# Optimization experiments

Hardware: AMD Instinct MI355X
Metric: run time of the kernel (lower is better)

The kernel has to match this reference:

```python
import jax, jax.numpy as jnp
import numpy as np

DIM = 2048
N_HEADS = 16
Q_LORA = 1536
KV_LORA = 512
NOPE = 128
ROPE = 64
V_HEAD = 128
QK_HEAD = NOPE + ROPE  # 192
B, S = 2, 2048
SCALE = QK_HEAD ** -0.5
EPS = 1e-6


def rmsnorm(x, w):
    return x * jax.lax.rsqrt(jnp.mean(x * x, axis=-1, keepdims=True) + EPS) * w


def apply_rope(x, cos, sin):
    # x: [b, s, h, d]; cos/sin: [s, d//2]; complex multiply on interleaved pairs
    xr = x.reshape(x.shape[:-1] + (-1, 2))
    c = cos[None, :, None, :]
    s = sin[None, :, None, :]
    re = xr[..., 0] * c - xr[..., 1] * s
    im = xr[..., 0] * s + xr[..., 1] * c
    return jnp.stack([re, im], axis=-1).reshape(x.shape)


def setup_inputs() -> dict:
    key = jax.random.key(0)
    ks = jax.random.split(key, 8)
    w = 0.02
    x = jax.random.normal(ks[0], (B, S, DIM), dtype=jnp.float32)
    # rotary tables
    inv_freq = 1.0 / (10000.0 ** (np.arange(0, ROPE, 2, dtype=np.float32) / ROPE))
    ang = np.arange(S, dtype=np.float32)[:, None] * inv_freq[None, :]
    freqs_cos = jnp.asarray(np.cos(ang))
    freqs_sin = jnp.asarray(np.sin(ang))
    # causal mask (upper triangular large-negative)
    mask = jnp.triu(jnp.full((S, S), -1e9, dtype=jnp.float32), k=1)
    return {
        "x": x,
        "freqs_cos": freqs_cos,
        "freqs_sin": freqs_sin,
        "mask": mask,
        "wq_a": w * jax.random.normal(ks[1], (Q_LORA, DIM), dtype=jnp.float32),
        "q_norm_w": jnp.ones((Q_LORA,), dtype=jnp.float32),
        "wq_b": w * jax.random.normal(ks[2], (N_HEADS * QK_HEAD, Q_LORA), dtype=jnp.float32),
        "wkv_a": w * jax.random.normal(ks[3], (KV_LORA + ROPE, DIM), dtype=jnp.float32),
        "kv_norm_w": jnp.ones((KV_LORA,), dtype=jnp.float32),
        "wkv_b": w * jax.random.normal(ks[4], (N_HEADS * (NOPE + V_HEAD), KV_LORA), dtype=jnp.float32),
        "wo": w * jax.random.normal(ks[5], (DIM, N_HEADS * V_HEAD), dtype=jnp.float32),
    }


def reference(x, freqs_cos, freqs_sin, mask, wq_a, q_norm_w, wq_b, wkv_a, kv_norm_w, wkv_b, wo):
    b, s, _ = x.shape
    # q low-rank path
    q = rmsnorm(x @ wq_a.T, q_norm_w) @ wq_b.T
    q = q.reshape(b, s, N_HEADS, QK_HEAD)
    q_nope, q_pe = q[..., :NOPE], q[..., NOPE:]
    q_pe = apply_rope(q_pe, freqs_cos, freqs_sin)
    # kv latent + decoupled rope key
    kv = x @ wkv_a.T
    c, k_pe = kv[..., :KV_LORA], kv[..., KV_LORA:]
    k_pe = apply_rope(k_pe[:, :, None, :], freqs_cos, freqs_sin)[:, :, 0, :]  # [b,t,r]
    # absorption: fold W^UK into q
    wkvb = wkv_b.reshape(N_HEADS, NOPE + V_HEAD, KV_LORA)
    q_abs = jnp.einsum("bshd,hdc->bshc", q_nope, wkvb[:, :NOPE])
    kv_cache = rmsnorm(c, kv_norm_w)  # [b,t,c] (start_pos=0 prefill)
    # scores over latent + rope parts, fp32 softmax
    scores = (jnp.einsum("bshc,btc->bsht", q_abs, kv_cache)
              + jnp.einsum("bshr,btr->bsht", q_pe, k_pe)) * SCALE
    scores = scores + mask[:, None, :]
    p = jax.nn.softmax(scores.astype(jnp.float32), axis=-1)
    # attend in latent space, then project out with W^UV
    o = jnp.einsum("bsht,btc->bshc", p, kv_cache)
    o = jnp.einsum("bshc,hdc->bshd", o, wkvb[:, -V_HEAD:])
    return o.reshape(b, s, N_HEADS * V_HEAD) @ wo.T
```

## Files before the change

kernel.cpp:

```cpp
#include <hip/hip_runtime.h>

typedef __bf16        bf16x8 __attribute__((ext_vector_type(8)));
typedef float         f32x4  __attribute__((ext_vector_type(4)));

typedef unsigned int __attribute__((address_space(1))) as1_u32;
typedef unsigned int __attribute__((address_space(3))) as3_u32;
#define ASYNC16(gp, lp) __builtin_amdgcn_global_load_lds((as1_u32*)(gp), (as3_u32*)(lp), 16, 0, 0)

#define SCALE_F 0.07216878364870323f
#define LOG2E_F 1.4426950408889634f
#define FQ (SCALE_F * LOG2E_F)

static __device__ __forceinline__ unsigned short f2bf(float f) {
  unsigned int u = __builtin_bit_cast(unsigned int, f);
  u += 0x7fff + ((u >> 16) & 1);
  return (unsigned short)(u >> 16);
}
static __device__ __forceinline__ float bf2f(unsigned short s) {
  unsigned int u = ((unsigned int)s) << 16;
  return __builtin_bit_cast(float, u);
}

__global__ __launch_bounds__(256) void k_f2b(const float* __restrict__ in,
                                             unsigned short* __restrict__ out, int n) {
  int stride = gridDim.x * 256;
  for (int i = blockIdx.x * 256 + threadIdx.x; i < n; i += stride) out[i] = f2bf(in[i]);
}

__global__ __launch_bounds__(256) void k_wkvb(const float* __restrict__ wkvb,
                                              unsigned short* __restrict__ w_nt,
                                              unsigned short* __restrict__ w_v) {
  int i = blockIdx.x * 256 + threadIdx.x;
  int h = i >> 16;
  int rem = i & 65535;
  int c = rem >> 7, d = rem & 127;
  w_nt[i] = f2bf(wkvb[((h << 8) + d) * 512 + c]);
  int d2 = rem >> 9, c2 = rem & 511;
  w_v[i] = f2bf(wkvb[((h << 8) + 128 + d2) * 512 + c2]);
}

template <int BF16_OUT>
__global__ __launch_bounds__(256) void k_gemm(
    const unsigned short* __restrict__ A, int lda, long long sA,
    const unsigned short* __restrict__ W, int ldw, long long sW,
    void* __restrict__ Cv, int ldc, long long sC, int K) {
  __shared__ unsigned short lA[128 * 32];
  __shared__ unsigned short lW[128 * 32];
  const int tid = threadIdx.x;
  const int lane = tid & 63;
  const int q4 = lane >> 4, c16 = lane & 15;
  const int wave = tid >> 6;
  const int wr = (wave >> 1) * 64, wc = (wave & 1) * 64;
  const int z = blockIdx.z;
  A += (long long)z * sA;
  W += (long long)z * sW;

  f32x4 acc[4][4];
#pragma unroll
  for (int i = 0; i < 4; i++)
#pragma unroll
    for (int j = 0; j < 4; j++) acc[i][j] = (f32x4)0.0f;

  const int r = tid >> 2;
  const int cc = (tid & 3) * 8;
  const unsigned short* gA0 = A + ((long long)blockIdx.y * 128 + r) * lda + cc;
  const unsigned short* gA1 = gA0 + (long long)64 * lda;
  const unsigned short* gW0 = W + ((long long)blockIdx.x * 128 + r) * ldw + cc;
  const unsigned short* gW1 = gW0 + (long long)64 * ldw;
  unsigned short* pA0 = &lA[r * 32 + cc];
  unsigned short* pA1 = &lA[(64 + r) * 32 + cc];
  unsigned short* pW0 = &lW[r * 32 + cc];
  unsigned short* pW1 = &lW[(64 + r) * 32 + cc];

  for (int k0 = 0; k0 < K; k0 += 32) {
    ASYNC16(gA0 + k0, pA0);
    ASYNC16(gA1 + k0, pA1);
    ASYNC16(gW0 + k0, pW0);
    ASYNC16(gW1 + k0, pW1);
    __syncthreads();
    bf16x8 af[4], wf[4];
#pragma unroll
    for (int mt = 0; mt < 4; mt++)
      af[mt] = *(const bf16x8*)&lA[(wr + mt * 16 + c16) * 32 + q4 * 8];
#pragma unroll
    for (int nt = 0; nt < 4; nt++)
      wf[nt] = *(const bf16x8*)&lW[(wc + nt * 16 + c16) * 32 + q4 * 8];
#pragma unroll
    for (int mt = 0; mt < 4; mt++)
#pragma unroll
      for (int nt = 0; nt < 4; nt++)
        acc[mt][nt] = __builtin_amdgcn_mfma_f32_16x16x32_bf16(af[mt], wf[nt], acc[mt][nt], 0, 0, 0);
    __syncthreads();
  }

  const long long row0 = (long long)blockIdx.y * 128 + wr + q4 * 4;
  const int col0 = blockIdx.x * 128 + wc + c16;
  if (BF16_OUT) {
    unsigned short* C = (unsigned short*)Cv + (long long)z * sC;
#pragma unroll
    for (int mt = 0; mt < 4; mt++)
#pragma unroll
      for (int i = 0; i < 4; i++) {
        long long rr = (row0 + mt * 16 + i) * (long long)ldc + col0;
#pragma unroll
        for (int nt = 0; nt < 4; nt++) C[rr + nt * 16] = f2bf(acc[mt][nt][i]);
      }
  } else {
    float* C = (float*)Cv + (long long)z * sC;
#pragma unroll
    for (int mt = 0; mt < 4; mt++)
#pragma unroll
      for (int i = 0; i < 4; i++) {
        long long rr = (row0 + mt * 16 + i) * (long long)ldc + col0;
#pragma unroll
        for (int nt = 0; nt < 4; nt++) C[rr + nt * 16] = acc[mt][nt][i];
      }
  }
}

__global__ __launch_bounds__(256) void k_rms_q(const float* __restrict__ in,
                                               const float* __restrict__ w,
                                               unsigned short* __restrict__ out) {
  const int row = blockIdx.x;
  const int tid = threadIdx.x;
  const float* x = in + (long long)row * 1536;
  float v[6], ss = 0.f;
#pragma unroll
  for (int i = 0; i < 6; i++) { v[i] = x[tid + i * 256]; ss += v[i] * v[i]; }
#pragma unroll
  for (int d = 1; d < 64; d <<= 1) ss += __shfl_xor(ss, d);
  __shared__ float red[4];
  if ((tid & 63) == 0) red[tid >> 6] = ss;
  __syncthreads();
  float sc = rsqrtf((red[0] + red[1] + red[2] + red[3]) * (1.0f / 1536.0f) + 1e-6f);
#pragma unroll
  for (int i = 0; i < 6; i++)
    out[(long long)row * 1536 + tid + i * 256] = f2bf(v[i] * sc * w[tid + i * 256]);
}

__global__ __launch_bounds__(256) void k_prep_kv(const float* __restrict__ kvf,
                                                 const float* __restrict__ wn,
                                                 const float* __restrict__ fc,
                                                 const float* __restrict__ fs,
                                                 unsigned short* __restrict__ kvk,
                                                 unsigned short* __restrict__ kvt) {
  const int row = blockIdx.x;
  const int tid = threadIdx.x;
  const float* x = kvf + (long long)row * 640;
  float v0 = x[tid], v1 = x[tid + 256];
  float ss = v0 * v0 + v1 * v1;
#pragma unroll
  for (int d = 1; d < 64; d <<= 1) ss += __shfl_xor(ss, d);
  __shared__ float red[4];
  if ((tid & 63) == 0) red[tid >> 6] = ss;
  __syncthreads();
  float sc = rsqrtf((red[0] + red[1] + red[2] + red[3]) * (1.0f / 512.0f) + 1e-6f);
  const int b = row >> 11, t = row & 2047, tt = t >> 5, tl = t & 31;
  float y0 = v0 * sc * wn[tid], y1 = v1 * sc * wn[tid + 256];
  unsigned short* kb = kvk + (long long)(b * 64 + tt) * 18432;
  unsigned short* vb = kvt + (long long)(b * 64 + tt) * 16384;
  const int d0 = tid, d1 = tid + 256;
  kb[((d0 >> 3) * 32 + tl) * 8 + (d0 & 7)] = f2bf(y0);
  kb[((d1 >> 3) * 32 + tl) * 8 + (d1 & 7)] = f2bf(y1);
  vb[((tl >> 3) * 512 + d0) * 8 + (tl & 7)] = f2bf(y0);
  vb[((tl >> 3) * 512 + d1) * 8 + (tl & 7)] = f2bf(y1);
  if (tid < 32) {
    float x0 = x[512 + 2 * tid], x1 = x[513 + 2 * tid];
    float c = fc[t * 32 + tid], s = fs[t * 32 + tid];
    const int e0 = 512 + 2 * tid, e1 = e0 + 1;
    kb[((e0 >> 3) * 32 + tl) * 8 + (e0 & 7)] = f2bf(x0 * c - x1 * s);
    kb[((e1 >> 3) * 32 + tl) * 8 + (e1 & 7)] = f2bf(x0 * s + x1 * c);
  }
}

__global__ __launch_bounds__(256) void k_repack(const unsigned short* __restrict__ q,
                                                const float* __restrict__ fc,
                                                const float* __restrict__ fs,
                                                unsigned short* __restrict__ qnp,
                                                unsigned short* __restrict__ qcat) {
  const int h = blockIdx.y;
  const int row = blockIdx.x * 4 + (threadIdx.x >> 6);
  const int ln = threadIdx.x & 63;
  const unsigned short* src = q + (long long)row * 3072 + h * 192;
  unsigned short* dn = qnp + ((long long)h * 4096 + row) * 128;
  dn[ln] = f2bf(bf2f(src[ln]) * FQ);
  dn[ln + 64] = f2bf(bf2f(src[ln + 64]) * FQ);
  if (ln < 32) {
    const int t = row & 2047;
    float x0 = bf2f(src[128 + 2 * ln]), x1 = bf2f(src[129 + 2 * ln]);
    float c = fc[t * 32 + ln], s = fs[t * 32 + ln];
    unsigned short* dc = qcat + ((long long)h * 4096 + row) * 576 + 512;
    dc[2 * ln] = f2bf((x0 * c - x1 * s) * FQ);
    dc[2 * ln + 1] = f2bf((x0 * s + x1 * c) * FQ);
  }
}

__global__ __launch_bounds__(256, 2) void k_attn(const unsigned short* __restrict__ qcat,
                                                 const unsigned short* __restrict__ kvk,
                                                 const unsigned short* __restrict__ kvt,
                                                 unsigned short* __restrict__ opk) {
  __shared__ unsigned short kt[18432];
  __shared__ unsigned short vt[16384];
  __shared__ unsigned short pl[4][16][32];
  const int tid = threadIdx.x, lane = tid & 63, wave = tid >> 6;
  const int q4 = lane >> 4, c16 = lane & 15;
  const int pair = blockIdx.x, h = blockIdx.y, b = blockIdx.z;
  const unsigned short* kvk_b = kvk + (long long)b * 64 * 18432;
  const unsigned short* kvt_b = kvt + (long long)b * 64 * 16384;

  bf16x8 ones;
#pragma unroll
  for (int i = 0; i < 8; i++) ones[i] = (__bf16)1.0f;

  for (int seg = 0; seg < 2; seg++) {
    const int qt = seg ? (31 - pair) : pair;
    const int s_wave = qt * 64 + wave * 16;
    const long long qrow = (long long)h * 4096 + b * 2048 + s_wave;

    bf16x8 qf[18];
    {
      const unsigned short* qp = qcat + (qrow + c16) * 576 + q4 * 8;
#pragma unroll
      for (int kc = 0; kc < 18; kc++) qf[kc] = *(const bf16x8*)(qp + kc * 32);
    }
    f32x4 oacc[32];
#pragma unroll
    for (int i = 0; i < 32; i++) oacc[i] = (f32x4)0.f;
    f32x4 lacc = (f32x4)0.f;

    const int nT = (qt + 1) * 2;
    for (int tt = 0; tt < nT; tt++) {
      const int t0 = tt * 32;
      const unsigned short* kg = kvk_b + (long long)tt * 18432;
      const unsigned short* vg = kvt_b + (long long)tt * 16384;
#pragma unroll
      for (int i = 0; i < 9; i++) { int ch = i * 256 + tid; ASYNC16(kg + ch * 8, &kt[ch * 8]); }
#pragma unroll
      for (int i = 0; i < 8; i++) { int ch = i * 256 + tid; ASYNC16(vg + ch * 8, &vt[ch * 8]); }
      __syncthreads();

      f32x4 s0 = (f32x4)0.f, s1 = (f32x4)0.f;
#pragma unroll
      for (int kc = 0; kc < 18; kc++) {
        const unsigned short* kp = &kt[((kc * 4 + q4) * 32 + c16) * 8];
        bf16x8 k0 = *(const bf16x8*)kp;
        bf16x8 k1 = *(const bf16x8*)(kp + 128);
        s0 = __builtin_amdgcn_mfma_f32_16x16x32_bf16(qf[kc], k0, s0, 0, 0, 0);
        s1 = __builtin_amdgcn_mfma_f32_16x16x32_bf16(qf[kc], k1, s1, 0, 0, 0);
      }

#pragma unroll
      for (int i = 0; i < 4; i++) {
        int s_g = s_wave + q4 * 4 + i;
        float v0 = (t0 + c16 > s_g) ? -3.0e38f : s0[i];
        float v1 = (t0 + 16 + c16 > s_g) ? -3.0e38f : s1[i];
        pl[wave][q4 * 4 + i][c16] = f2bf(exp2f(v0));
        pl[wave][q4 * 4 + i][16 + c16] = f2bf(exp2f(v1));
      }
      bf16x8 pf = *(const bf16x8*)&pl[wave][c16][q4 * 8];

      lacc = __builtin_amdgcn_mfma_f32_16x16x32_bf16(pf, ones, lacc, 0, 0, 0);
#pragma unroll
      for (int ct = 0; ct < 32; ct++) {
        bf16x8 vv = *(const bf16x8*)&vt[(q4 * 512 + ct * 16 + c16) * 8];
        oacc[ct] = __builtin_amdgcn_mfma_f32_16x16x32_bf16(pf, vv, oacc[ct], 0, 0, 0);
      }
      __syncthreads();
    }

    const long long orow = qrow + q4 * 4;
#pragma unroll
    for (int i = 0; i < 4; i++) {
      float inv = 1.0f / lacc[i];
      unsigned short* dst = opk + (orow + i) * 512;
#pragma unroll
      for (int ct = 0; ct < 32; ct++) dst[ct * 16 + c16] = f2bf(oacc[ct][i] * inv);
    }
  }
}

extern "C" void kernel_launch(void* const* d_in, const int* in_sizes, int n_in,
                              void* d_out, int out_size, void* d_ws, size_t ws_size,
                              hipStream_t stream) {
  (void)in_sizes; (void)n_in; (void)out_size; (void)ws_size;
  const float* x     = (const float*)d_in[0];
  const float* fc    = (const float*)d_in[1];
  const float* fs    = (const float*)d_in[2];
  const float* wq_a  = (const float*)d_in[4];
  const float* qnw   = (const float*)d_in[5];
  const float* wq_b  = (const float*)d_in[6];
  const float* wkv_a = (const float*)d_in[7];
  const float* kvnw  = (const float*)d_in[8];
  const float* wkv_b = (const float*)d_in[9];
  const float* wo    = (const float*)d_in[10];
  float* out = (float*)d_out;
  char* ws = (char*)d_ws;

  const size_t O_WQA  = 0;
  const size_t O_WQB  = 6291456;
  const size_t O_WKVA = 15728640;
  const size_t O_WNT  = 18350080;
  const size_t O_WV   = 20447232;
  const size_t O_WO   = 22544384;
  const size_t O_RA   = 30932992;
  const size_t O_RB   = 47710208;
  const size_t O_QAN  = 72876032;
  const size_t O_KVF  = 85458944;
  const size_t O_KVK  = 95944704;
  const size_t O_KVT  = 100663296;
  const size_t O_QCAT = 104857600;
  const size_t O_OPK  = 180355072;

  unsigned short* W_QA = (unsigned short*)(ws + O_WQA);
  unsigned short* W_QB = (unsigned short*)(ws + O_WQB);
  unsigned short* W_KVA = (unsigned short*)(ws + O_WKVA);
  unsigned short* W_NT = (unsigned short*)(ws + O_WNT);
  unsigned short* W_V  = (unsigned short*)(ws + O_WV);
  unsigned short* W_O  = (unsigned short*)(ws + O_WO);
  unsigned short* X_B  = (unsigned short*)(ws + O_RA);
  unsigned short* QNP  = (unsigned short*)(ws + O_RA);
  unsigned short* OPC  = (unsigned short*)(ws + O_RA);
  float*          QA_F = (float*)(ws + O_RB);
  unsigned short* QB   = (unsigned short*)(ws + O_RB);
  unsigned short* QAN  = (unsigned short*)(ws + O_QAN);
  float*          KV_F = (float*)(ws + O_KVF);
  unsigned short* KVK  = (unsigned short*)(ws + O_KVK);
  unsigned short* KVT  = (unsigned short*)(ws + O_KVT);
  unsigned short* QCAT = (unsigned short*)(ws + O_QCAT);
  unsigned short* OPK  = (unsigned short*)(ws + O_OPK);

  dim3 blk(256);
  k_f2b<<<dim3(4096), blk, 0, stream>>>(x, X_B, 4096 * 2048);
  k_f2b<<<dim3(1024), blk, 0, stream>>>(wq_a, W_QA, 1536 * 2048);
  k_f2b<<<dim3(1024), blk, 0, stream>>>(wq_b, W_QB, 3072 * 1536);
  k_f2b<<<dim3(1024), blk, 0, stream>>>(wkv_a, W_KVA, 576 * 2048);
  k_f2b<<<dim3(1024), blk, 0, stream>>>(wo, W_O, 2048 * 2048);
  k_wkvb<<<dim3(4096), blk, 0, stream>>>(wkv_b, W_NT, W_V);

  k_gemm<0><<<dim3(12, 32, 1), blk, 0, stream>>>(X_B, 2048, 0, W_QA, 2048, 0, QA_F, 1536, 0, 2048);
  k_gemm<0><<<dim3(5, 32, 1), blk, 0, stream>>>(X_B, 2048, 0, W_KVA, 2048, 0, KV_F, 640, 0, 2048);
  k_rms_q<<<dim3(4096), blk, 0, stream>>>(QA_F, qnw, QAN);
  k_prep_kv<<<dim3(4096), blk, 0, stream>>>(KV_F, kvnw, fc, fs, KVK, KVT);
  k_gemm<1><<<dim3(24, 32, 1), blk, 0, stream>>>(QAN, 1536, 0, W_QB, 1536, 0, QB, 3072, 0, 1536);
  k_repack<<<dim3(1024, 16), blk, 0, stream>>>(QB, fc, fs, QNP, QCAT);
  k_gemm<1><<<dim3(4, 32, 16), blk, 0, stream>>>(QNP, 128, 4096LL * 128, W_NT, 128, 512LL * 128,
                                                 QCAT, 576, 4096LL * 576, 128);
  k_attn<<<dim3(16, 16, 2), blk, 0, stream>>>(QCAT, KVK, KVT, OPK);
  k_gemm<1><<<dim3(1, 32, 16), blk, 0, stream>>>(OPK, 512, 4096LL * 512, W_V, 512, 128LL * 512,
                                                 OPC, 2048, 128, 512);
  k_gemm<0><<<dim3(16, 32, 1), blk, 0, stream>>>(OPC, 2048, 0, W_O, 2048, 0, out, 2048, 0, 2048);
}
```

Measured before the change: 696.6 us.

## Switch attention to 32x32 MFMA tiles with 128-row query blocks and double-buffered KV

Reworks the MLA attention kernel to use 32x32x16 MFMA instructions, with each wave owning 32 query rows so a block covers 128 rows. The KV tiles are double-buffered in LDS and the next tile is prefetched asynchronously while the current one is computed. Masking is now applied only on diagonal tiles, and the grid is halved to match. The intent is better reuse of each KV tile loaded into LDS and hiding load latency. The cost is roughly doubled LDS and register pressure, which drops occupancy to one block per CU and leaves only 512 blocks in the grid.

After: 737.2 us. +5.8%, slower.

```diff
diff --git a/kernel.cpp b/kernel.cpp
--- a/kernel.cpp
+++ b/kernel.cpp
@@ -2,6 +2,7 @@
 
 typedef __bf16        bf16x8 __attribute__((ext_vector_type(8)));
 typedef float         f32x4  __attribute__((ext_vector_type(4)));
+typedef float         f32x16 __attribute__((ext_vector_type(16)));
 
 typedef unsigned int __attribute__((address_space(1))) as1_u32;
 typedef unsigned int __attribute__((address_space(3))) as3_u32;
@@ -195,15 +196,15 @@
   }
 }
 
-__global__ __launch_bounds__(256, 2) void k_attn(const unsigned short* __restrict__ qcat,
+__global__ __launch_bounds__(256, 1) void k_attn(const unsigned short* __restrict__ qcat,
                                                  const unsigned short* __restrict__ kvk,
                                                  const unsigned short* __restrict__ kvt,
                                                  unsigned short* __restrict__ opk) {
-  __shared__ unsigned short kt[18432];
-  __shared__ unsigned short vt[16384];
-  __shared__ unsigned short pl[4][16][32];
+  __shared__ unsigned short kt[2][18432];
+  __shared__ unsigned short vt[2][16384];
+  __shared__ unsigned short pl[4][32][36];
   const int tid = threadIdx.x, lane = tid & 63, wave = tid >> 6;
-  const int q4 = lane >> 4, c16 = lane & 15;
+  const int m32 = lane & 31, half = lane >> 5;
   const int pair = blockIdx.x, h = blockIdx.y, b = blockIdx.z;
   const unsigned short* kvk_b = kvk + (long long)b * 64 * 18432;
   const unsigned short* kvt_b = kvt + (long long)b * 64 * 16384;
@@ -213,68 +214,81 @@
   for (int i = 0; i < 8; i++) ones[i] = (__bf16)1.0f;
 
   for (int seg = 0; seg < 2; seg++) {
-    const int qt = seg ? (31 - pair) : pair;
-    const int s_wave = qt * 64 + wave * 16;
+    const int qt = seg ? (15 - pair) : pair;
+    const int s_wave = qt * 128 + wave * 32;
     const long long qrow = (long long)h * 4096 + b * 2048 + s_wave;
 
-    bf16x8 qf[18];
+    bf16x8 qf[36];
     {
-      const unsigned short* qp = qcat + (qrow + c16) * 576 + q4 * 8;
-#pragma unroll
-      for (int kc = 0; kc < 18; kc++) qf[kc] = *(const bf16x8*)(qp + kc * 32);
+      const unsigned short* qp = qcat + (qrow + m32) * 576 + half * 8;
+#pragma unroll
+      for (int ks = 0; ks < 36; ks++) qf[ks] = *(const bf16x8*)(qp + ks * 16);
     }
-    f32x4 oacc[32];
-#pragma unroll
-    for (int i = 0; i < 32; i++) oacc[i] = (f32x4)0.f;
-    f32x4 lacc = (f32x4)0.f;
-
-    const int nT = (qt + 1) * 2;
+    f32x16 oacc[16];
+#pragma unroll
+    for (int i = 0; i < 16; i++) oacc[i] = (f32x16)0.f;
+    f32x16 lacc = (f32x16)0.f;
+
+    const int nT = (qt + 1) * 4;
+    {
+      const unsigned short* kg = kvk_b;
+      const unsigned short* vg = kvt_b;
+#pragma unroll
+      for (int i = 0; i < 9; i++) { int ch = i * 256 + tid; ASYNC16(kg + ch * 8, &kt[0][ch * 8]); }
+#pragma unroll
+      for (int i = 0; i < 8; i++) { int ch = i * 256 + tid; ASYNC16(vg + ch * 8, &vt[0][ch * 8]); }
+    }
+    __syncthreads();
+
     for (int tt = 0; tt < nT; tt++) {
+      const int cur = tt & 1;
+      if (tt + 1 < nT) {
+        const unsigned short* kg = kvk_b + (long long)(tt + 1) * 18432;
+        const unsigned short* vg = kvt_b + (long long)(tt + 1) * 16384;
+#pragma unroll
+        for (int i = 0; i < 9; i++) { int ch = i * 256 + tid; ASYNC16(kg + ch * 8, &kt[cur ^ 1][ch * 8]); }
+#pragma unroll
+        for (int i = 0; i < 8; i++) { int ch = i * 256 + tid; ASYNC16(vg + ch * 8, &vt[cur ^ 1][ch * 8]); }
+      }
       const int t0 = tt * 32;
-      const unsigned short* kg = kvk_b + (long long)tt * 18432;
-      const unsigned short* vg = kvt_b + (long long)tt * 16384;
-#pragma unroll
-      for (int i = 0; i < 9; i++) { int ch = i * 256 + tid; ASYNC16(kg + ch * 8, &kt[ch * 8]); }
-#pragma unroll
-      for (int i = 0; i < 8; i++) { int ch = i * 256 + tid; ASYNC16(vg + ch * 8, &vt[ch * 8]); }
-      __syncthreads();
-
-      f32x4 s0 = (f32x4)0.f, s1 = (f32x4)0.f;
-#pragma unroll
-      for (int kc = 0; kc < 18; kc++) {
-        const unsigned short* kp = &kt[((kc * 4 + q4) * 32 + c16) * 8];
-        bf16x8 k0 = *(const bf16x8*)kp;
-        bf16x8 k1 = *(const bf16x8*)(kp + 128);
-        s0 = __builtin_amdgcn_mfma_f32_16x16x32_bf16(qf[kc], k0, s0, 0, 0, 0);
-        s1 = __builtin_amdgcn_mfma_f32_16x16x32_bf16(qf[kc], k1, s1, 0, 0, 0);
-      }
-
-#pragma unroll
-      for (int i = 0; i < 4; i++) {
-        int s_g = s_wave + q4 * 4 + i;
-        float v0 = (t0 + c16 > s_g) ? -3.0e38f : s0[i];
-        float v1 = (t0 + 16 + c16 > s_g) ? -3.0e38f : s1[i];
-        pl[wave][q4 * 4 + i][c16] = f2bf(exp2f(v0));
-        pl[wave][q4 * 4 + i][16 + c16] = f2bf(exp2f(v1));
-      }
-      bf16x8 pf = *(const bf16x8*)&pl[wave][c16][q4 * 8];
-
-      lacc = __builtin_amdgcn_mfma_f32_16x16x32_bf16(pf, ones, lacc, 0, 0, 0);
-#pragma unroll
-      for (int ct = 0; ct < 32; ct++) {
-        bf16x8 vv = *(const bf16x8*)&vt[(q4 * 512 + ct * 16 + c16) * 8];
-        oacc[ct] = __builtin_amdgcn_mfma_f32_16x16x32_bf16(pf, vv, oacc[ct], 0, 0, 0);
+
+      f32x16 sacc = (f32x16)0.f;
+#pragma unroll
+      for (int ks = 0; ks < 36; ks++) {
+        bf16x8 kf = *(const bf16x8*)&kt[cur][((ks * 2 + half) * 32 + m32) * 8];
+        sacc = __builtin_amdgcn_mfma_f32_32x32x16_bf16(qf[ks], kf, sacc, 0, 0, 0);
+      }
+
+      const bool needmask = (t0 + 31 > s_wave);
+#pragma unroll
+      for (int r = 0; r < 16; r++) {
+        int row = (r & 3) + 4 * half + 8 * (r >> 2);
+        float v = sacc[r];
+        if (needmask && (t0 + m32 > s_wave + row)) v = -3.0e38f;
+        pl[wave][row][m32] = f2bf(exp2f(v));
+      }
+      bf16x8 pf0 = *(const bf16x8*)&pl[wave][m32][half * 8];
+      bf16x8 pf1 = *(const bf16x8*)&pl[wave][m32][16 + half * 8];
+
+      lacc = __builtin_amdgcn_mfma_f32_32x32x16_bf16(pf0, ones, lacc, 0, 0, 0);
+      lacc = __builtin_amdgcn_mfma_f32_32x32x16_bf16(pf1, ones, lacc, 0, 0, 0);
+#pragma unroll
+      for (int ct = 0; ct < 16; ct++) {
+        bf16x8 v0 = *(const bf16x8*)&vt[cur][((half) * 512 + ct * 32 + m32) * 8];
+        bf16x8 v1 = *(const bf16x8*)&vt[cur][((2 + half) * 512 + ct * 32 + m32) * 8];
+        oacc[ct] = __builtin_amdgcn_mfma_f32_32x32x16_bf16(pf0, v0, oacc[ct], 0, 0, 0);
+        oacc[ct] = __builtin_amdgcn_mfma_f32_32x32x16_bf16(pf1, v1, oacc[ct], 0, 0, 0);
       }
       __syncthreads();
     }
 
-    const long long orow = qrow + q4 * 4;
-#pragma unroll
-    for (int i = 0; i < 4; i++) {
-      float inv = 1.0f / lacc[i];
-      unsigned short* dst = opk + (orow + i) * 512;
-#pragma unroll
-      for (int ct = 0; ct < 32; ct++) dst[ct * 16 + c16] = f2bf(oacc[ct][i] * inv);
+#pragma unroll
+    for (int r = 0; r < 16; r++) {
+      int row = (r & 3) + 4 * half + 8 * (r >> 2);
+      float inv = 1.0f / lacc[r];
+      unsigned short* dst = opk + (qrow + row) * 512 + m32;
+#pragma unroll
+      for (int ct = 0; ct < 16; ct++) dst[ct * 32] = f2bf(oacc[ct][r] * inv);
     }
   }
 }
@@ -345,7 +359,7 @@
   k_repack<<<dim3(1024, 16), blk, 0, stream>>>(QB, fc, fs, QNP, QCAT);
   k_gemm<1><<<dim3(4, 32, 16), blk, 0, stream>>>(QNP, 128, 4096LL * 128, W_NT, 128, 512LL * 128,
                                                  QCAT, 576, 4096LL * 576, 128);
-  k_attn<<<dim3(16, 16, 2), blk, 0, stream>>>(QCAT, KVK, KVT, OPK);
+  k_attn<<<dim3(8, 16, 2), blk, 0, stream>>>(QCAT, KVK, KVT, OPK);
   k_gemm<1><<<dim3(1, 32, 16), blk, 0, stream>>>(OPK, 512, 4096LL * 512, W_V, 512, 128LL * 512,
                                                  OPC, 2048, 128, 512);
   k_gemm<0><<<dim3(16, 32, 1), blk, 0, stream>>>(OPC, 2048, 0, W_O, 2048, 0, out, 2048, 0, 2048);
```

## Double-buffer 16-key K tiles in attention and prefetch next tile during compute

Applied to the files above, without the earlier changes.

The packed K layout changes from 32-key tiles to 16-key tiles, and the attention loop now steps over 16 keys at a time. The next K tile is prefetched into a second LDS buffer while the current one is used, and V is loaded every other step so its copy overlaps the score computation. Probabilities are packed in pairs with a lane shuffle and written as 32-bit stores, and the PV MFMAs run once per 32 keys. This aims to hide global-to-LDS latency, at the cost of twice as many loop iterations and barriers.

Result: slower. 732.8 us (+5.2%).

```diff
diff --git a/kernel.cpp b/kernel.cpp
--- a/kernel.cpp
+++ b/kernel.cpp
@@ -155,21 +155,23 @@
   if ((tid & 63) == 0) red[tid >> 6] = ss;
   __syncthreads();
   float sc = rsqrtf((red[0] + red[1] + red[2] + red[3]) * (1.0f / 512.0f) + 1e-6f);
-  const int b = row >> 11, t = row & 2047, tt = t >> 5, tl = t & 31;
+  const int b = row >> 11, t = row & 2047;
+  const int kt16 = t >> 4, kl = t & 15;
+  const int vt32 = t >> 5, vl = t & 31;
   float y0 = v0 * sc * wn[tid], y1 = v1 * sc * wn[tid + 256];
-  unsigned short* kb = kvk + (long long)(b * 64 + tt) * 18432;
-  unsigned short* vb = kvt + (long long)(b * 64 + tt) * 16384;
+  unsigned short* kb = kvk + (long long)(b * 128 + kt16) * 9216;
+  unsigned short* vb = kvt + (long long)(b * 64 + vt32) * 16384;
   const int d0 = tid, d1 = tid + 256;
-  kb[((d0 >> 3) * 32 + tl) * 8 + (d0 & 7)] = f2bf(y0);
-  kb[((d1 >> 3) * 32 + tl) * 8 + (d1 & 7)] = f2bf(y1);
-  vb[((tl >> 3) * 512 + d0) * 8 + (tl & 7)] = f2bf(y0);
-  vb[((tl >> 3) * 512 + d1) * 8 + (tl & 7)] = f2bf(y1);
+  kb[((d0 >> 3) * 16 + kl) * 8 + (d0 & 7)] = f2bf(y0);
+  kb[((d1 >> 3) * 16 + kl) * 8 + (d1 & 7)] = f2bf(y1);
+  vb[((vl >> 3) * 512 + d0) * 8 + (vl & 7)] = f2bf(y0);
+  vb[((vl >> 3) * 512 + d1) * 8 + (vl & 7)] = f2bf(y1);
   if (tid < 32) {
     float x0 = x[512 + 2 * tid], x1 = x[513 + 2 * tid];
     float c = fc[t * 32 + tid], s = fs[t * 32 + tid];
     const int e0 = 512 + 2 * tid, e1 = e0 + 1;
-    kb[((e0 >> 3) * 32 + tl) * 8 + (e0 & 7)] = f2bf(x0 * c - x1 * s);
-    kb[((e1 >> 3) * 32 + tl) * 8 + (e1 & 7)] = f2bf(x0 * s + x1 * c);
+    kb[((e0 >> 3) * 16 + kl) * 8 + (e0 & 7)] = f2bf(x0 * c - x1 * s);
+    kb[((e1 >> 3) * 16 + kl) * 8 + (e1 & 7)] = f2bf(x0 * s + x1 * c);
   }
 }
 
@@ -199,13 +201,13 @@
                                                  const unsigned short* __restrict__ kvk,
                                                  const unsigned short* __restrict__ kvt,
                                                  unsigned short* __restrict__ opk) {
-  __shared__ unsigned short kt[18432];
+  __shared__ unsigned short kt[2][9216];
   __shared__ unsigned short vt[16384];
   __shared__ unsigned short pl[4][16][32];
   const int tid = threadIdx.x, lane = tid & 63, wave = tid >> 6;
   const int q4 = lane >> 4, c16 = lane & 15;
   const int pair = blockIdx.x, h = blockIdx.y, b = blockIdx.z;
-  const unsigned short* kvk_b = kvk + (long long)b * 64 * 18432;
+  const unsigned short* kvk_b = kvk + (long long)b * 128 * 9216;
   const unsigned short* kvt_b = kvt + (long long)b * 64 * 16384;
 
   bf16x8 ones;
@@ -228,42 +230,60 @@
     for (int i = 0; i < 32; i++) oacc[i] = (f32x4)0.f;
     f32x4 lacc = (f32x4)0.f;
 
-    const int nT = (qt + 1) * 2;
-    for (int tt = 0; tt < nT; tt++) {
-      const int t0 = tt * 32;
-      const unsigned short* kg = kvk_b + (long long)tt * 18432;
-      const unsigned short* vg = kvt_b + (long long)tt * 16384;
-#pragma unroll
-      for (int i = 0; i < 9; i++) { int ch = i * 256 + tid; ASYNC16(kg + ch * 8, &kt[ch * 8]); }
-#pragma unroll
-      for (int i = 0; i < 8; i++) { int ch = i * 256 + tid; ASYNC16(vg + ch * 8, &vt[ch * 8]); }
-      __syncthreads();
-
-      f32x4 s0 = (f32x4)0.f, s1 = (f32x4)0.f;
-#pragma unroll
-      for (int kc = 0; kc < 18; kc++) {
-        const unsigned short* kp = &kt[((kc * 4 + q4) * 32 + c16) * 8];
-        bf16x8 k0 = *(const bf16x8*)kp;
-        bf16x8 k1 = *(const bf16x8*)(kp + 128);
-        s0 = __builtin_amdgcn_mfma_f32_16x16x32_bf16(qf[kc], k0, s0, 0, 0, 0);
-        s1 = __builtin_amdgcn_mfma_f32_16x16x32_bf16(qf[kc], k1, s1, 0, 0, 0);
-      }
-
+    const int nT = (qt + 1) * 4;
+
+#pragma unroll
+    for (int i = 0; i < 5; i++) {
+      int ch = i * 256 + tid;
+      if (ch < 1152) ASYNC16(kvk_b + ch * 8, &kt[0][ch * 8]);
+    }
+    __syncthreads();
+
+    for (int t = 0; t < nT; t++) {
+      const int cur = t & 1;
+      if (t + 1 < nT) {
+        const unsigned short* kg = kvk_b + (long long)(t + 1) * 9216;
+#pragma unroll
+        for (int i = 0; i < 5; i++) {
+          int ch = i * 256 + tid;
+          if (ch < 1152) ASYNC16(kg + ch * 8, &kt[cur ^ 1][ch * 8]);
+        }
+      }
+      if (!(t & 1)) {
+        const unsigned short* vg = kvt_b + (long long)(t >> 1) * 16384;
+#pragma unroll
+        for (int i = 0; i < 8; i++) {
+          int ch = i * 256 + tid;
+          ASYNC16(vg + ch * 8, &vt[ch * 8]);
+        }
+      }
+
+      f32x4 sacc = (f32x4)0.f;
+#pragma unroll
+      for (int ks = 0; ks < 18; ks++) {
+        bf16x8 kf = *(const bf16x8*)&kt[cur][((ks * 4 + q4) * 16 + c16) * 8];
+        sacc = __builtin_amdgcn_mfma_f32_16x16x32_bf16(qf[ks], kf, sacc, 0, 0, 0);
+      }
+
+      const int tc0 = t * 16;
 #pragma unroll
       for (int i = 0; i < 4; i++) {
         int s_g = s_wave + q4 * 4 + i;
-        float v0 = (t0 + c16 > s_g) ? -3.0e38f : s0[i];
-        float v1 = (t0 + 16 + c16 > s_g) ? -3.0e38f : s1[i];
-        pl[wave][q4 * 4 + i][c16] = f2bf(exp2f(v0));
-        pl[wave][q4 * 4 + i][16 + c16] = f2bf(exp2f(v1));
-      }
-      bf16x8 pf = *(const bf16x8*)&pl[wave][c16][q4 * 8];
-
-      lacc = __builtin_amdgcn_mfma_f32_16x16x32_bf16(pf, ones, lacc, 0, 0, 0);
-#pragma unroll
-      for (int ct = 0; ct < 32; ct++) {
-        bf16x8 vv = *(const bf16x8*)&vt[(q4 * 512 + ct * 16 + c16) * 8];
-        oacc[ct] = __builtin_amdgcn_mfma_f32_16x16x32_bf16(pf, vv, oacc[ct], 0, 0, 0);
+        float v = (tc0 + c16 > s_g) ? -3.0e38f : sacc[i];
+        unsigned int u = f2bf(exp2f(v));
+        unsigned int o = (unsigned int)__shfl_xor((int)u, 1);
+        unsigned int w32 = (lane & 1) ? ((u << 16) | o) : ((o << 16) | u);
+        if (!(lane & 1)) *(unsigned int*)&pl[wave][q4 * 4 + i][cur * 16 + c16] = w32;
+      }
+
+      if (t & 1) {
+        bf16x8 pf = *(const bf16x8*)&pl[wave][c16][q4 * 8];
+        lacc = __builtin_amdgcn_mfma_f32_16x16x32_bf16(pf, ones, lacc, 0, 0, 0);
+#pragma unroll
+        for (int ct = 0; ct < 32; ct++) {
+          bf16x8 vv = *(const bf16x8*)&vt[(q4 * 512 + ct * 16 + c16) * 8];
+          oacc[ct] = __builtin_amdgcn_mfma_f32_16x16x32_bf16(pf, vv, oacc[ct], 0, 0, 0);
+        }
       }
       __syncthreads();
     }
```
